# Kernel optimization log

Hardware: AMD Instinct MI355X
Metric: run time of the kernel (lower is better)

## Reference

```python
import jax, jax.numpy as jnp
import numpy as np

DR_SAMP = 1.0
NEWTON_STEPSIZE = 1.0
MAX_STEP = 1.0
TERM_EPS = 1e-4
TERM_DELTA_EPS = 1e-2


def _path_eval(pts, r):
    """Piecewise-linear closed path sampled uniformly at DR_SAMP.
    Returns (point, unit_tangent, unit_normal) at arclength r."""
    N = pts.shape[0]
    L = N * DR_SAMP
    u = jnp.mod(r, L) / DR_SAMP            # fractional segment index
    i0 = jnp.floor(u).astype(jnp.int32) % N
    i1 = (i0 + 1) % N                      # closed-path wraparound
    frac = (u - jnp.floor(u))[..., None]
    p0, p1 = pts[i0], pts[i1]
    point = p0 + frac * (p1 - p0)
    tang = (p1 - p0) / DR_SAMP
    tang = tang / jnp.linalg.norm(tang, axis=-1, keepdims=True)
    norm = jnp.stack([-tang[..., 1], tang[..., 0]], axis=-1)  # 90deg CCW rotation
    return point, tang, norm


def _interp(vals, r, N):
    """Linear interpolation of per-sample values on the uniform arclength grid."""
    L = N * DR_SAMP
    u = jnp.mod(r, L) / DR_SAMP
    i0 = jnp.floor(u).astype(jnp.int32) % N
    i1 = (i0 + 1) % N
    frac = u - jnp.floor(u)
    return vals[i0] * (1.0 - frac) + vals[i1] * frac


def setup_inputs() -> dict:
    key = jax.random.key(0)
    k1, k2, k3, k4, k5 = jax.random.split(key, 5)
    N, B = 8192, 32768
    L = N * DR_SAMP
    R = L / (2.0 * np.pi)  # circle radius so circumference == L (uniform arclength sampling)
    theta = 2.0 * jnp.pi * jnp.arange(N, dtype=jnp.float32) / N
    refline_points = R * jnp.stack([jnp.cos(theta), jnp.sin(theta)], axis=-1)
    left_widths = 4.0 + 4.0 * jax.random.uniform(k1, (N,), dtype=jnp.float32)
    right_widths = 4.0 + 4.0 * jax.random.uniform(k2, (N,), dtype=jnp.float32)
    # query positions scattered near the track: random arclength + lateral offset
    s = L * jax.random.uniform(k3, (B,), dtype=jnp.float32)
    lat = 3.0 * jax.random.normal(k4, (B,), dtype=jnp.float32)
    ang = 2.0 * jnp.pi * s / L
    positions = (R + lat)[:, None] * jnp.stack([jnp.cos(ang), jnp.sin(ang)], axis=-1)
    positions = positions + 0.1 * jax.random.normal(k5, (B, 2), dtype=jnp.float32)
    return {"positions": positions, "refline_points": refline_points,
            "left_widths": left_widths, "right_widths": right_widths,
            "newton_iterations": 8}


def reference(positions, refline_points, left_widths, right_widths, newton_iterations):
    N = refline_points.shape[0]
    L = N * DR_SAMP
    arclengths = jnp.arange(N, dtype=positions.dtype) * DR_SAMP
    # KD-tree closest sampled point -> brute-force argmin over squared distances
    d2 = (jnp.sum(positions * positions, -1, keepdims=True)
          - 2.0 * positions @ refline_points.T
          + jnp.sum(refline_points * refline_points, -1))  # [B, N]
    r = arclengths[jnp.argmin(d2, axis=-1)]                 # [B]
    # Newton refinement of arclength parameter (fixed iteration count, masked termination)
    done = jnp.zeros(r.shape, dtype=bool)
    for _ in range(int(newton_iterations)):
        point, tang, _ = _path_eval(refline_points, r)
        delta = positions - point
        fprime = -jnp.sum(delta * tang, axis=-1)            # d/dr 0.5|p(r)-x|^2 (unit speed => f''=1)
        step = jnp.clip(-fprime, -MAX_STEP, MAX_STEP)
        r = jnp.mod(r + jnp.where(done, 0.0, NEWTON_STEPSIZE * step), L)
        done = done | (jnp.abs(fprime) < TERM_EPS) | (jnp.abs(step) < TERM_DELTA_EPS)
    point, tang, norm = _path_eval(refline_points, r)
    deltas = positions - point
    normal_projections = jnp.sum(deltas * norm, axis=-1)
    left_width_vals = _interp(left_widths, r, N)
    right_width_vals = _interp(right_widths, r, N)
    return (r, point, tang, norm, deltas, normal_projections, left_width_vals, right_width_vals)
```

## Files before the change

### kernel.cpp

```cpp
#include <hip/hip_runtime.h>
#include <math.h>


#define DR_SAMP 1.0f
#define MAX_STEP 1.0f
#define TERM_EPS 1e-4f
#define TERM_DELTA_EPS 1e-2f

#define COARSE 32
#define WIN 64
#define BLK 256
#define LPQ 16

#define IDXBITS 13
#define IDXMASK ((1u << IDXBITS) - 1u)
#define KEYMASK (~IDXMASK)

__device__ __forceinline__ unsigned int pack_key(float d2, int i) {
    return (__float_as_uint(d2) & KEYMASK) | (unsigned int)i;
}

__device__ __forceinline__ int wrapN(int i, int N) {
    return (i < 0) ? i + N : ((i >= N) ? i - N : i);
}

__device__ __forceinline__ unsigned int grp16_min(unsigned int k) {
    k = min(k, (unsigned int)__shfl_xor((int)k, 1));
    k = min(k, (unsigned int)__shfl_xor((int)k, 2));
    k = min(k, (unsigned int)__shfl_xor((int)k, 4));
    k = min(k, (unsigned int)__shfl_xor((int)k, 8));
    return k;
}

__global__ __launch_bounds__(BLK, 8) void bc_fused(
    const float* __restrict__ pos, const float* __restrict__ ref,
    const float* __restrict__ lw, const float* __restrict__ rw,
    const int* __restrict__ nit_p, float* __restrict__ out, int B, int N)
{
    __shared__ float2 scoarse[512];

    const float2* __restrict__ ref2 = (const float2*)ref;
    int NC = N / COARSE;

    for (int t = threadIdx.x; t < NC; t += BLK)
        scoarse[t] = ref2[t * COARSE];
    __syncthreads();

    int gtid = blockIdx.x * BLK + threadIdx.x;
    int q = gtid / LPQ;
    int l = threadIdx.x & (LPQ - 1);
    if (q >= B) return;

    const float L = (float)N * DR_SAMP;
    float px = pos[2 * q], py = pos[2 * q + 1];

    unsigned int c0 = 0xFFFFFFFFu, c1 = 0xFFFFFFFFu;
    unsigned int c2 = 0xFFFFFFFFu, c3 = 0xFFFFFFFFu;
#define CANDC(pt, ii, acc)                                   \
    {                                                        \
        float dx_ = px - (pt).x, dy_ = py - (pt).y;          \
        float d2_ = fmaf(dx_, dx_, dy_ * dy_);               \
        acc = min(acc, pack_key(d2_, (ii)));                 \
    }
    for (int m = l; m + 3 * LPQ < NC; m += 4 * LPQ) {
        float2 a0 = scoarse[m];
        float2 a1 = scoarse[m + LPQ];
        float2 a2 = scoarse[m + 2 * LPQ];
        float2 a3 = scoarse[m + 3 * LPQ];
        CANDC(a0, m * COARSE, c0)
        CANDC(a1, (m + LPQ) * COARSE, c1)
        CANDC(a2, (m + 2 * LPQ) * COARSE, c2)
        CANDC(a3, (m + 3 * LPQ) * COARSE, c3)
    }
#undef CANDC
    int jc = (int)(grp16_min(min(min(c0, c1), min(c2, c3))) & IDXMASK);

    unsigned int fbest = 0xFFFFFFFFu;
    int base = jc - (WIN / 2 - 1);
#pragma unroll
    for (int t = 0; t < WIN / LPQ; ++t) {
        int i0 = wrapN(base + l + t * LPQ, N);
        float2 p0v = ref2[i0];
        float dx0 = px - p0v.x, dy0 = py - p0v.y;
        fbest = min(fbest, pack_key(fmaf(dx0, dx0, dy0 * dy0), i0));
    }
    fbest = grp16_min(fbest);
    float r = (float)(int)(fbest & IDXMASK) * DR_SAMP;

    int niter = nit_p[0];
    bool done = false;
    for (int it = 0; it < niter; ++it) {
        float fu = floorf(r);
        int i0 = (int)fu;
        if (i0 >= N) i0 -= N;
        int i1 = i0 + 1;
        if (i1 >= N) i1 -= N;
        float frac = r - fu;
        float2 p0 = ref2[i0];
        float2 p1 = ref2[i1];
        float ex = p1.x - p0.x, ey = p1.y - p0.y;
        float ptx = fmaf(frac, ex, p0.x);
        float pty = fmaf(frac, ey, p0.y);
        float inv = rsqrtf(fmaf(ex, ex, ey * ey));
        float tx = ex * inv, ty = ey * inv;
        float dx = px - ptx, dy = py - pty;
        float fprime = -(dx * tx + dy * ty);
        float step = fminf(fmaxf(-fprime, -MAX_STEP), MAX_STEP);
        if (!done) {
            r += step;
            if (r >= L) r -= L;
            if (r < 0.0f) r += L;
        }
        done = done || (fabsf(fprime) < TERM_EPS) || (fabsf(step) < TERM_DELTA_EPS);
    }

    if (l != 0) return;

    float fu = floorf(r);
    int i0 = (int)fu;
    if (i0 >= N) i0 -= N;
    int i1 = i0 + 1;
    if (i1 >= N) i1 -= N;
    float frac = r - fu;
    float2 p0 = ref2[i0];
    float2 p1 = ref2[i1];
    float ex = p1.x - p0.x, ey = p1.y - p0.y;
    float ptx = fmaf(frac, ex, p0.x);
    float pty = fmaf(frac, ey, p0.y);
    float inv = rsqrtf(fmaf(ex, ex, ey * ey));
    float tx = ex * inv;
    float ty = ey * inv;
    float nx = -ty, ny = tx;
    float dx = px - ptx, dy = py - pty;
    float proj = dx * nx + dy * ny;
    float lv = lw[i0] * (1.0f - frac) + lw[i1] * frac;
    float rv = rw[i0] * (1.0f - frac) + rw[i1] * frac;

    out[q] = r;
    *(float2*)(out + B + 2 * q)     = make_float2(ptx, pty);
    *(float2*)(out + 3 * B + 2 * q) = make_float2(tx, ty);
    *(float2*)(out + 5 * B + 2 * q) = make_float2(nx, ny);
    *(float2*)(out + 7 * B + 2 * q) = make_float2(dx, dy);
    out[9 * B + q]  = proj;
    out[10 * B + q] = lv;
    out[11 * B + q] = rv;
}

extern "C" void kernel_launch(void* const* d_in, const int* in_sizes, int n_in,
                              void* d_out, int out_size, void* d_ws, size_t ws_size,
                              hipStream_t stream) {
    const float* pos = (const float*)d_in[0];
    const float* ref = (const float*)d_in[1];
    const float* lw  = (const float*)d_in[2];
    const float* rw  = (const float*)d_in[3];
    const int*   nit = (const int*)d_in[4];
    int B = in_sizes[0] / 2;
    int N = in_sizes[1] / 2;
    float* out = (float*)d_out;

    long long threads = (long long)B * LPQ;
    int nb = (int)((threads + BLK - 1) / BLK);
    bc_fused<<<nb, BLK, 0, stream>>>(pos, ref, lw, rw, nit, out, B, N);
}
```

Before: 70.89 us.

## Prepack refline into segment-pair float4 arrays via a small pre-kernel

Adds a pre-pass kernel that packs each segment's endpoints, and the adjacent left/right widths, into float4 workspace arrays. It also packs the coarse samples two per float4. The main kernel now reads the coarse samples straight from global memory instead of staging them in shared memory behind a block barrier. Newton steps and the final evaluation each do one 16-byte load instead of two 8-byte loads plus wrap logic. The cost is an extra kernel launch and workspace traffic, and the coarse scan now relies on the cache instead of LDS.

```diff
diff --git a/kernel.cpp b/kernel.cpp
--- a/kernel.cpp
+++ b/kernel.cpp
@@ -32,20 +32,32 @@
     return k;
 }
 
+__global__ __launch_bounds__(256) void bc_pack(
+    const float* __restrict__ ref, const float* __restrict__ lw,
+    const float* __restrict__ rw, float4* __restrict__ pairs,
+    float4* __restrict__ wpair, float4* __restrict__ coarse4, int N)
+{
+    int i = blockIdx.x * 256 + threadIdx.x;
+    const float2* __restrict__ ref2 = (const float2*)ref;
+    if (i < N) {
+        int i1 = (i + 1 == N) ? 0 : i + 1;
+        float2 a = ref2[i], b = ref2[i1];
+        pairs[i] = make_float4(a.x, a.y, b.x, b.y);
+        wpair[i] = make_float4(lw[i], lw[i1], rw[i], rw[i1]);
+    }
+    int NC2 = N / (2 * COARSE);
+    if (i < NC2) {
+        float2 a = ref2[(2 * i) * COARSE];
+        float2 b = ref2[(2 * i + 1) * COARSE];
+        coarse4[i] = make_float4(a.x, a.y, b.x, b.y);
+    }
+}
+
 __global__ __launch_bounds__(BLK, 8) void bc_fused(
-    const float* __restrict__ pos, const float* __restrict__ ref,
-    const float* __restrict__ lw, const float* __restrict__ rw,
+    const float* __restrict__ pos, const float4* __restrict__ pairs,
+    const float4* __restrict__ wpair, const float4* __restrict__ coarse4,
     const int* __restrict__ nit_p, float* __restrict__ out, int B, int N)
 {
-    __shared__ float2 scoarse[512];
-
-    const float2* __restrict__ ref2 = (const float2*)ref;
-    int NC = N / COARSE;
-
-    for (int t = threadIdx.x; t < NC; t += BLK)
-        scoarse[t] = ref2[t * COARSE];
-    __syncthreads();
-
     int gtid = blockIdx.x * BLK + threadIdx.x;
     int q = gtid / LPQ;
     int l = threadIdx.x & (LPQ - 1);
@@ -54,35 +66,34 @@
     const float L = (float)N * DR_SAMP;
     float px = pos[2 * q], py = pos[2 * q + 1];
 
+    int NCP = N / (2 * COARSE);
     unsigned int c0 = 0xFFFFFFFFu, c1 = 0xFFFFFFFFu;
-    unsigned int c2 = 0xFFFFFFFFu, c3 = 0xFFFFFFFFu;
-#define CANDC(pt, ii, acc)                                   \
-    {                                                        \
-        float dx_ = px - (pt).x, dy_ = py - (pt).y;          \
-        float d2_ = fmaf(dx_, dx_, dy_ * dy_);               \
-        acc = min(acc, pack_key(d2_, (ii)));                 \
+    for (int j = l; j < NCP; j += 2 * LPQ) {
+        float4 pa = coarse4[j];
+        float4 pb = coarse4[j + LPQ];
+        int ma = 2 * j * COARSE, mb = 2 * (j + LPQ) * COARSE;
+        float dxa = px - pa.x, dya = py - pa.y;
+        float dxb = px - pa.z, dyb = py - pa.w;
+        c0 = min(c0, pack_key(fmaf(dxa, dxa, dya * dya), ma));
+        c1 = min(c1, pack_key(fmaf(dxb, dxb, dyb * dyb), ma + COARSE));
+        float dxc = px - pb.x, dyc = py - pb.y;
+        float dxd = px - pb.z, dyd = py - pb.w;
+        c0 = min(c0, pack_key(fmaf(dxc, dxc, dyc * dyc), mb));
+        c1 = min(c1, pack_key(fmaf(dxd, dxd, dyd * dyd), mb + COARSE));
     }
-    for (int m = l; m + 3 * LPQ < NC; m += 4 * LPQ) {
-        float2 a0 = scoarse[m];
-        float2 a1 = scoarse[m + LPQ];
-        float2 a2 = scoarse[m + 2 * LPQ];
-        float2 a3 = scoarse[m + 3 * LPQ];
-        CANDC(a0, m * COARSE, c0)
-        CANDC(a1, (m + LPQ) * COARSE, c1)
-        CANDC(a2, (m + 2 * LPQ) * COARSE, c2)
-        CANDC(a3, (m + 3 * LPQ) * COARSE, c3)
-    }
-#undef CANDC
-    int jc = (int)(grp16_min(min(min(c0, c1), min(c2, c3))) & IDXMASK);
+    int jc = (int)(grp16_min(min(c0, c1)) & IDXMASK);
 
     unsigned int fbest = 0xFFFFFFFFu;
     int base = jc - (WIN / 2 - 1);
 #pragma unroll
-    for (int t = 0; t < WIN / LPQ; ++t) {
-        int i0 = wrapN(base + l + t * LPQ, N);
-        float2 p0v = ref2[i0];
-        float dx0 = px - p0v.x, dy0 = py - p0v.y;
-        fbest = min(fbest, pack_key(fmaf(dx0, dx0, dy0 * dy0), i0));
+    for (int t = 0; t < 2; ++t) {
+        int ia = wrapN(base + 2 * l + t * 2 * LPQ, N);
+        int ib = (ia + 1 == N) ? 0 : ia + 1;
+        float4 pr = pairs[ia];
+        float dxa = px - pr.x, dya = py - pr.y;
+        float dxb = px - pr.z, dyb = py - pr.w;
+        fbest = min(fbest, pack_key(fmaf(dxa, dxa, dya * dya), ia));
+        fbest = min(fbest, pack_key(fmaf(dxb, dxb, dyb * dyb), ib));
     }
     fbest = grp16_min(fbest);
     float r = (float)(int)(fbest & IDXMASK) * DR_SAMP;
@@ -93,14 +104,11 @@
         float fu = floorf(r);
         int i0 = (int)fu;
         if (i0 >= N) i0 -= N;
-        int i1 = i0 + 1;
-        if (i1 >= N) i1 -= N;
         float frac = r - fu;
-        float2 p0 = ref2[i0];
-        float2 p1 = ref2[i1];
-        float ex = p1.x - p0.x, ey = p1.y - p0.y;
-        float ptx = fmaf(frac, ex, p0.x);
-        float pty = fmaf(frac, ey, p0.y);
+        float4 pr = pairs[i0];
+        float ex = pr.z - pr.x, ey = pr.w - pr.y;
+        float ptx = fmaf(frac, ex, pr.x);
+        float pty = fmaf(frac, ey, pr.y);
         float inv = rsqrtf(fmaf(ex, ex, ey * ey));
         float tx = ex * inv, ty = ey * inv;
         float dx = px - ptx, dy = py - pty;
@@ -119,22 +127,20 @@
     float fu = floorf(r);
     int i0 = (int)fu;
     if (i0 >= N) i0 -= N;
-    int i1 = i0 + 1;
-    if (i1 >= N) i1 -= N;
     float frac = r - fu;
-    float2 p0 = ref2[i0];
-    float2 p1 = ref2[i1];
-    float ex = p1.x - p0.x, ey = p1.y - p0.y;
-    float ptx = fmaf(frac, ex, p0.x);
-    float pty = fmaf(frac, ey, p0.y);
+    float4 pr = pairs[i0];
+    float4 wp = wpair[i0];
+    float ex = pr.z - pr.x, ey = pr.w - pr.y;
+    float ptx = fmaf(frac, ex, pr.x);
+    float pty = fmaf(frac, ey, pr.y);
     float inv = rsqrtf(fmaf(ex, ex, ey * ey));
     float tx = ex * inv;
     float ty = ey * inv;
     float nx = -ty, ny = tx;
     float dx = px - ptx, dy = py - pty;
     float proj = dx * nx + dy * ny;
-    float lv = lw[i0] * (1.0f - frac) + lw[i1] * frac;
-    float rv = rw[i0] * (1.0f - frac) + rw[i1] * frac;
+    float lv = wp.x * (1.0f - frac) + wp.y * frac;
+    float rv = wp.z * (1.0f - frac) + wp.w * frac;
 
     out[q] = r;
     *(float2*)(out + B + 2 * q)     = make_float2(ptx, pty);
@@ -158,7 +164,14 @@
     int N = in_sizes[1] / 2;
     float* out = (float*)d_out;
 
+    float4* pairs   = (float4*)d_ws;
+    float4* wpair   = pairs + N;
+    float4* coarse4 = wpair + N;
+
+    int nbp = (N + 255) / 256;
+    bc_pack<<<nbp, 256, 0, stream>>>(ref, lw, rw, pairs, wpair, coarse4, N);
+
     long long threads = (long long)B * LPQ;
     int nb = (int)((threads + BLK - 1) / BLK);
-    bc_fused<<<nb, BLK, 0, stream>>>(pos, ref, lw, rw, nit, out, B, N);
+    bc_fused<<<nb, BLK, 0, stream>>>(pos, pairs, wpair, coarse4, nit, out, B, N);
 }
```

Measured after the change: 70.78 us. Within noise of the previous version (-0.2%).
